# Kernel optimization log

Hardware: AMD Instinct MI355X
Metric: run time of the kernel (lower is better)

## Reference

```python
import jax, jax.numpy as jnp
import numpy as np

TEMP = 0.3

def setup_inputs() -> dict:
    key = jax.random.key(0)
    k1, k2, k3 = jax.random.split(key, 3)
    N, d, T, Q = 2048, 256, 256, 64
    scale = 1.0 / np.sqrt(d)  # keep dot/temp in a numerically safe range for exp
    x = jax.random.normal(k1, (N, d), jnp.float32) * scale
    y = jax.random.normal(k2, (T, Q, d), jnp.float32) * scale
    track_idxs = jax.random.randint(k3, (N,), 0, T, dtype=jnp.int32)
    return {"x": x, "track_idxs": track_idxs, "y": y}


def reference(x, track_idxs, y):
    # Defaults: global_contrast=True, separate_tracks=True, static_contrast=True,
    # soft_condition=True, sim_type='dot'. Vectorized segment-sum form of the
    # per-unique-track Python loop in the original module.
    T, Q, d = y.shape
    yf = y.reshape(T * Q, d)                       # flatten(0,1): track-major
    y_idxs = jnp.tile(jnp.arange(T, dtype=jnp.int32), Q)  # torch .repeat(Q) == tile
    tid = track_idxs.astype(jnp.int32)

    S_xy = jnp.exp(x @ yf.T / TEMP)                # [N, T*Q]
    S_xx = jnp.exp(x @ x.T / TEMP)                 # [N, N]

    # Sum S columns grouped by (buggy-but-faithful) y track id / x track id -> [N, T]
    xy_by_track = jax.ops.segment_sum(S_xy.T, y_idxs, num_segments=T).T
    xx_by_track = jax.ops.segment_sum(S_xx.T, tid, num_segments=T).T

    rxy_total = S_xy.sum(axis=1)                   # [N]
    rxx_total = S_xx.sum(axis=1)                   # [N]
    rxy_pos = jnp.take_along_axis(xy_by_track, tid[:, None], axis=1)[:, 0]
    rxx_pos_full = jnp.take_along_axis(xx_by_track, tid[:, None], axis=1)[:, 0]
    rxx_pos = rxx_pos_full - jnp.diagonal(S_xx)    # exclude self-pairs (1 - eye)

    # per-row numerator/denominator contributions
    num_i = rxy_pos + 0.5 * rxx_pos                # static same-track sum halved
    den_i = (rxy_total - rxy_pos) + (rxx_total - rxx_pos_full)

    num_t = jax.ops.segment_sum(num_i, tid, num_segments=T)  # [T]
    den_t = jax.ops.segment_sum(den_i, tid, num_segments=T)
    counts = jax.ops.segment_sum(jnp.ones_like(num_i), tid, num_segments=T)
    present = counts > 0                            # unique() track ids

    num_safe = jnp.where(present, num_t, 1.0)
    den_safe = jnp.where(present, den_t, 0.0)
    loss_t = -jnp.log(num_safe / (den_safe + num_safe))  # soft_condition loss
    loss_t = jnp.where(present, loss_t, 0.0)
    n_present = present.sum().astype(loss_t.dtype)
    return (loss_t.sum() / n_present).reshape(1)
```

## Files before the change

### kernel.cpp

```cpp
#include <hip/hip_runtime.h>

#define NN   2048
#define DD   256
#define TT   256
#define NYC  16384
#define CHUNK_COLS 128
#define NCHUNK_XY 128
#define NCHUNK_XX 16
#define NROWBLK   16

static constexpr float INV_TEMP = 1.0f / 0.3f;

typedef __bf16 bf16x8 __attribute__((ext_vector_type(8)));
typedef float  f32x4  __attribute__((ext_vector_type(4)));


__global__ void cvt_zero_kernel(const float* __restrict__ x, const float* __restrict__ y,
                                bf16x8* __restrict__ xfl, bf16x8* __restrict__ yfl,
                                float* __restrict__ acc ) {
    const int tid0   = blockIdx.x * blockDim.x + threadIdx.x;
    const int stride = gridDim.x * blockDim.x;
    for (int j = tid0; j < 3 * NN; j += stride) acc[j] = 0.f;

    const int NXF = NN * DD / 8;
    for (int j = tid0; j < NXF; j += stride) {
        const int gk  = j >> 6;
        const int sub = j & 63;
        const int qq  = sub & 3;
        const int cc  = (sub >> 2) & 15;
        const int col = ((gk >> 3) << 4) + cc;
        const int k0  = ((gk & 7) << 5) + (qq << 3);
        const float4* s = (const float4*)(x + (size_t)col * DD + k0);
        float4 v0 = s[0], v1 = s[1];
        bf16x8 o;
        o[0] = (__bf16)v0.x; o[1] = (__bf16)v0.y; o[2] = (__bf16)v0.z; o[3] = (__bf16)v0.w;
        o[4] = (__bf16)v1.x; o[5] = (__bf16)v1.y; o[6] = (__bf16)v1.z; o[7] = (__bf16)v1.w;
        xfl[(size_t)gk * 64 + qq * 16 + cc] = o;
    }
    const int NYF = NYC * DD / 8;
    for (int j = tid0; j < NYF; j += stride) {
        const int gk  = j >> 6;
        const int sub = j & 63;
        const int qq  = sub & 3;
        const int cc  = (sub >> 2) & 15;
        const int col = ((gk >> 3) << 4) + cc;
        const int k0  = ((gk & 7) << 5) + (qq << 3);
        const float4* s = (const float4*)(y + (size_t)col * DD + k0);
        float4 v0 = s[0], v1 = s[1];
        bf16x8 o;
        o[0] = (__bf16)v0.x; o[1] = (__bf16)v0.y; o[2] = (__bf16)v0.z; o[3] = (__bf16)v0.w;
        o[4] = (__bf16)v1.x; o[5] = (__bf16)v1.y; o[6] = (__bf16)v1.z; o[7] = (__bf16)v1.w;
        yfl[(size_t)gk * 64 + qq * 16 + cc] = o;
    }
}

__global__ __launch_bounds__(256, 3) void stats_kernel(
        const bf16x8* __restrict__ xfl, const bf16x8* __restrict__ yfl,
        const int* __restrict__ tid,
        float* __restrict__ Tot, float* __restrict__ Pxy,
        float* __restrict__ Pxx, float* __restrict__ diag) {
    __shared__ __align__(16) char bstage[2][8192];

    const int id    = blockIdx.x;
    const int chunk = (id & 7) + ((id >> 7) << 3);
    const int bx    = (id >> 3) & 15;
    const int mode  = (chunk >= NCHUNK_XY);
    const int colbase = (mode ? chunk - NCHUNK_XY : chunk) * CHUNK_COLS;
    const bf16x8* __restrict__ colfl = mode ? xfl : yfl;

    const int tix  = threadIdx.x;
    const int lane = tix & 63;
    const int w    = tix >> 6;
    const int c16  = lane & 15;
    const int q    = lane >> 4;
    const int rowbase = bx * 128 + w * 32;
    const int rowg    = rowbase >> 4;

    bf16x8 a[2][8];
#pragma unroll
    for (int t = 0; t < 2; t++)
#pragma unroll
        for (int ks = 0; ks < 8; ks++)
            a[t][ks] = xfl[((size_t)(rowg + t) * 8 + ks) * 64 + lane];

    int trow[2];
#pragma unroll
    for (int t = 0; t < 2; t++) {
        const int rb = rowbase + t * 16 + q * 4;
        trow[t] = tid[rb] | (tid[rb + 1] << 8) | (tid[rb + 2] << 16) | (tid[rb + 3] << 24);
    }

    int ctid[8];
#pragma unroll
    for (int ct = 0; ct < 8; ct++) {
        const int col = colbase + ct * 16 + c16;
        ctid[ct] = mode ? tid[col] : (col & (TT - 1));
    }

    const char* gbase = (const char*)colfl + ((size_t)(colbase >> 4)) * 8192 + tix * 16;
    const bool wantdiag = mode && (bx == (colbase >> 7));

    float tot[2][4] = {};
    float pos[2][4] = {};

#define STAGE(ct_, buf_)                                                              \
    do {                                                                              \
        const char* g_ = gbase + (size_t)(ct_) * 8192;                                \
        __builtin_amdgcn_global_load_lds(                                             \
            (const __attribute__((address_space(1))) void*)g_,                        \
            (__attribute__((address_space(3))) void*)&bstage[buf_][tix * 16],         \
            16, 0, 0);                                                                \
        __builtin_amdgcn_global_load_lds(                                             \
            (const __attribute__((address_space(1))) void*)(g_ + 4096),               \
            (__attribute__((address_space(3))) void*)&bstage[buf_][4096 + tix * 16],  \
            16, 0, 0);                                                                \
    } while (0)

    STAGE(0, 0);
    __syncthreads();

#pragma unroll
    for (int ct = 0; ct < 8; ct++) {
        if (ct < 7) STAGE(ct + 1, (ct + 1) & 1);
        const char* lbase = &bstage[ct & 1][0];

        f32x4 acc0 = {0.f, 0.f, 0.f, 0.f};
        f32x4 acc1 = {0.f, 0.f, 0.f, 0.f};
#pragma unroll
        for (int h = 0; h < 2; h++) {
            bf16x8 bf[4];
#pragma unroll
            for (int k = 0; k < 4; k++)
                bf[k] = *(const bf16x8*)(lbase + (h * 4 + k) * 1024 + lane * 16);
#pragma unroll
            for (int k = 0; k < 4; k++) {
                acc0 = __builtin_amdgcn_mfma_f32_16x16x32_bf16(a[0][h * 4 + k], bf[k], acc0, 0, 0, 0);
                acc1 = __builtin_amdgcn_mfma_f32_16x16x32_bf16(a[1][h * 4 + k], bf[k], acc1, 0, 0, 0);
            }
        }

        const int col = colbase + ct * 16 + c16;
#pragma unroll
        for (int t = 0; t < 2; t++) {
            const f32x4 acv = t ? acc1 : acc0;
            const int rw0 = rowbase + t * 16 + q * 4;
#pragma unroll
            for (int r = 0; r < 4; r++) {
                const float val = __expf(acv[r] * INV_TEMP);
                tot[t][r] += val;
                pos[t][r] += (((trow[t] >> (8 * r)) & 255) == ctid[ct]) ? val : 0.f;
                if (wantdiag && col == rw0 + r) diag[col] = val;
            }
        }
        __syncthreads();
    }
#undef STAGE

#pragma unroll
    for (int t = 0; t < 2; t++)
#pragma unroll
        for (int r = 0; r < 4; r++) {
            float aS = tot[t][r], p = pos[t][r];
#pragma unroll
            for (int off = 1; off < 16; off <<= 1) {
                aS += __shfl_xor(aS, off);
                p  += __shfl_xor(p, off);
            }
            if (c16 == 0) {
                const int row = rowbase + t * 16 + q * 4 + r;
                atomicAdd(&Tot[row], aS);
                atomicAdd(mode ? &Pxx[row] : &Pxy[row], p);
            }
        }
}

__global__ void finalize_kernel(const float* __restrict__ Tot, const float* __restrict__ Pxy,
                                const float* __restrict__ Pxx, const float* __restrict__ diag,
                                const int* __restrict__ tid, float* __restrict__ out) {
    __shared__ float num_s[TT], den_s[TT];
    __shared__ int cnt_s[TT];
    const int t = threadIdx.x;
    num_s[t] = 0.f; den_s[t] = 0.f; cnt_s[t] = 0;
    __syncthreads();
    for (int i = t; i < NN; i += 256) {
        float tt_ = Tot[i], pxy = Pxy[i], pxx = Pxx[i];
        float num = pxy + 0.5f * (pxx - diag[i]);
        float den = tt_ - pxy - pxx;
        int tr = tid[i];
        atomicAdd(&num_s[tr], num);
        atomicAdd(&den_s[tr], den);
        atomicAdd(&cnt_s[tr], 1);
    }
    __syncthreads();
    float lt = 0.f, pr = 0.f;
    if (cnt_s[t] > 0) {
        lt = -logf(num_s[t] / (den_s[t] + num_s[t]));
        pr = 1.f;
    }
    for (int off = 32; off; off >>= 1) { lt += __shfl_down(lt, off); pr += __shfl_down(pr, off); }
    __shared__ float ls[4], ps[4];
    if ((t & 63) == 0) { ls[t >> 6] = lt; ps[t >> 6] = pr; }
    __syncthreads();
    if (t == 0) out[0] = (ls[0] + ls[1] + ls[2] + ls[3]) / (ps[0] + ps[1] + ps[2] + ps[3]);
}

extern "C" void kernel_launch(void* const* d_in, const int* in_sizes, int n_in,
                              void* d_out, int out_size, void* d_ws, size_t ws_size,
                              hipStream_t stream) {
    const float* x   = (const float*)d_in[0];
    const int*   tid = (const int*)d_in[1];
    const float* y   = (const float*)d_in[2];
    float* out = (float*)d_out;

    char* ws = (char*)d_ws;
    bf16x8* xfl = (bf16x8*)ws;
    bf16x8* yfl = (bf16x8*)(ws + (1u << 20));
    float* acc  = (float*)(ws + 9u * (1u << 20));
    float* Tot  = acc;
    float* Pxy  = acc + NN;
    float* Pxx  = acc + 2 * NN;
    float* diag = acc + 3 * NN;

    cvt_zero_kernel<<<2304, 256, 0, stream>>>(x, y, xfl, yfl, acc);
    stats_kernel<<<NROWBLK * (NCHUNK_XY + NCHUNK_XX), 256, 0, stream>>>(
        xfl, yfl, tid, Tot, Pxy, Pxx, diag);
    finalize_kernel<<<1, 256, 0, stream>>>(Tot, Pxy, Pxx, diag, tid, out);
}
```

Before: 113.5 us.

## Deepen stats kernel LDS prefetch pipeline to four stages with explicit vmcnt waits

The column-tile staging buffer grows from double to quadruple buffering. Three tiles are prefetched before the A-fragment and track-id loads, and each later tile is issued three steps ahead. The loop is unrolled by hand, and the full `__syncthreads` is replaced by an explicit `s_waitcnt vmcnt` plus a raw barrier. The aim is to hide more global-to-LDS latency behind the MFMA/exp work. In exchange, LDS use per block doubles to 32KB, and correctness now depends on hand-tuned vmcnt counts.

```diff
diff --git a/kernel.cpp b/kernel.cpp
--- a/kernel.cpp
+++ b/kernel.cpp
@@ -59,7 +59,7 @@
         const int* __restrict__ tid,
         float* __restrict__ Tot, float* __restrict__ Pxy,
         float* __restrict__ Pxx, float* __restrict__ diag) {
-    __shared__ __align__(16) char bstage[2][8192];
+    __shared__ __align__(16) char bstage[4][8192];
 
     const int id    = blockIdx.x;
     const int chunk = (id & 7) + ((id >> 7) << 3);
@@ -76,6 +76,26 @@
     const int rowbase = bx * 128 + w * 32;
     const int rowg    = rowbase >> 4;
 
+    const char* gbase = (const char*)colfl + ((size_t)(colbase >> 4)) * 8192 + tix * 16;
+    const bool wantdiag = mode && (bx == (colbase >> 7));
+
+#define STAGE(ct_)                                                                        \
+    do {                                                                                  \
+        const char* g_ = gbase + (size_t)(ct_) * 8192;                                    \
+        __builtin_amdgcn_global_load_lds(                                                 \
+            (const __attribute__((address_space(1))) void*)g_,                            \
+            (__attribute__((address_space(3))) void*)&bstage[(ct_) & 3][tix * 16],        \
+            16, 0, 0);                                                                    \
+        __builtin_amdgcn_global_load_lds(                                                 \
+            (const __attribute__((address_space(1))) void*)(g_ + 4096),                   \
+            (__attribute__((address_space(3))) void*)&bstage[(ct_) & 3][4096 + tix * 16], \
+            16, 0, 0);                                                                    \
+    } while (0)
+#define WAITV(n_) asm volatile("s_waitcnt vmcnt(" #n_ ")" ::: "memory")
+#define BAR() __builtin_amdgcn_s_barrier()
+
+    STAGE(0); STAGE(1); STAGE(2);
+
     bf16x8 a[2][8];
 #pragma unroll
     for (int t = 0; t < 2; t++)
@@ -97,64 +117,58 @@
         ctid[ct] = mode ? tid[col] : (col & (TT - 1));
     }
 
-    const char* gbase = (const char*)colfl + ((size_t)(colbase >> 4)) * 8192 + tix * 16;
-    const bool wantdiag = mode && (bx == (colbase >> 7));
-
     float tot[2][4] = {};
     float pos[2][4] = {};
 
-#define STAGE(ct_, buf_)                                                              \
-    do {                                                                              \
-        const char* g_ = gbase + (size_t)(ct_) * 8192;                                \
-        __builtin_amdgcn_global_load_lds(                                             \
-            (const __attribute__((address_space(1))) void*)g_,                        \
-            (__attribute__((address_space(3))) void*)&bstage[buf_][tix * 16],         \
-            16, 0, 0);                                                                \
-        __builtin_amdgcn_global_load_lds(                                             \
-            (const __attribute__((address_space(1))) void*)(g_ + 4096),               \
-            (__attribute__((address_space(3))) void*)&bstage[buf_][4096 + tix * 16],  \
-            16, 0, 0);                                                                \
+#define COMPUTE(ct_)                                                                       \
+    do {                                                                                   \
+        const char* lbase = &bstage[(ct_) & 3][0];                                         \
+        f32x4 acc0 = {0.f, 0.f, 0.f, 0.f};                                                 \
+        f32x4 acc1 = {0.f, 0.f, 0.f, 0.f};                                                 \
+        _Pragma("unroll")                                                                  \
+        for (int h = 0; h < 2; h++) {                                                      \
+            bf16x8 bf[4];                                                                  \
+            _Pragma("unroll")                                                              \
+            for (int k = 0; k < 4; k++)                                                    \
+                bf[k] = *(const bf16x8*)(lbase + (h * 4 + k) * 1024 + lane * 16);          \
+            _Pragma("unroll")                                                              \
+            for (int k = 0; k < 4; k++) {                                                  \
+                acc0 = __builtin_amdgcn_mfma_f32_16x16x32_bf16(a[0][h * 4 + k], bf[k],     \
+                                                               acc0, 0, 0, 0);             \
+                acc1 = __builtin_amdgcn_mfma_f32_16x16x32_bf16(a[1][h * 4 + k], bf[k],     \
+                                                               acc1, 0, 0, 0);             \
+            }                                                                              \
+        }                                                                                  \
+        const int col = colbase + (ct_) * 16 + c16;                                        \
+        _Pragma("unroll")                                                                  \
+        for (int t = 0; t < 2; t++) {                                                      \
+            const f32x4 acv = t ? acc1 : acc0;                                             \
+            const int rw0 = rowbase + t * 16 + q * 4;                                      \
+            _Pragma("unroll")                                                              \
+            for (int r = 0; r < 4; r++) {                                                  \
+                const float val = __expf(acv[r] * INV_TEMP);                               \
+                tot[t][r] += val;                                                          \
+                pos[t][r] += (((trow[t] >> (8 * r)) & 255) == ctid[(ct_)]) ? val : 0.f;    \
+                if (wantdiag && col == rw0 + r) diag[col] = val;                           \
+            }                                                                              \
+        }                                                                                  \
     } while (0)
 
-    STAGE(0, 0);
-    __syncthreads();
-
-#pragma unroll
-    for (int ct = 0; ct < 8; ct++) {
-        if (ct < 7) STAGE(ct + 1, (ct + 1) & 1);
-        const char* lbase = &bstage[ct & 1][0];
-
-        f32x4 acc0 = {0.f, 0.f, 0.f, 0.f};
-        f32x4 acc1 = {0.f, 0.f, 0.f, 0.f};
-#pragma unroll
-        for (int h = 0; h < 2; h++) {
-            bf16x8 bf[4];
-#pragma unroll
-            for (int k = 0; k < 4; k++)
-                bf[k] = *(const bf16x8*)(lbase + (h * 4 + k) * 1024 + lane * 16);
-#pragma unroll
-            for (int k = 0; k < 4; k++) {
-                acc0 = __builtin_amdgcn_mfma_f32_16x16x32_bf16(a[0][h * 4 + k], bf[k], acc0, 0, 0, 0);
-                acc1 = __builtin_amdgcn_mfma_f32_16x16x32_bf16(a[1][h * 4 + k], bf[k], acc1, 0, 0, 0);
-            }
-        }
-
-        const int col = colbase + ct * 16 + c16;
-#pragma unroll
-        for (int t = 0; t < 2; t++) {
-            const f32x4 acv = t ? acc1 : acc0;
-            const int rw0 = rowbase + t * 16 + q * 4;
-#pragma unroll
-            for (int r = 0; r < 4; r++) {
-                const float val = __expf(acv[r] * INV_TEMP);
-                tot[t][r] += val;
-                pos[t][r] += (((trow[t] >> (8 * r)) & 255) == ctid[ct]) ? val : 0.f;
-                if (wantdiag && col == rw0 + r) diag[col] = val;
-            }
-        }
-        __syncthreads();
-    }
+    WAITV(4); BAR();
+
+    STAGE(3); COMPUTE(0); WAITV(4); BAR();
+    STAGE(4); COMPUTE(1); WAITV(4); BAR();
+    STAGE(5); COMPUTE(2); WAITV(4); BAR();
+    STAGE(6); COMPUTE(3); WAITV(4); BAR();
+    STAGE(7); COMPUTE(4); WAITV(4); BAR();
+    COMPUTE(5); WAITV(2); BAR();
+    COMPUTE(6); WAITV(0); BAR();
+    COMPUTE(7);
+
+#undef COMPUTE
 #undef STAGE
+#undef WAITV
+#undef BAR
 
 #pragma unroll
     for (int t = 0; t < 2; t++)
```

Result: faster. 109.2 us (-3.7%).
